# Optimization experiments

Hardware: AMD Instinct MI355X
Metric: run time of the kernel (lower is better)

## Reference

```python
import jax, jax.numpy as jnp
import numpy as np

NUM_HEAD = 16
DIM = 1024
T, B = 2048, 4


def setup_inputs() -> dict:
    key = jax.random.key(0)
    ks = jax.random.split(key, 12)
    s = 1.0 / np.sqrt(DIM)
    return {
        "x1": jax.random.normal(ks[0], (T, B, DIM), jnp.float32),
        "x2": jax.random.normal(ks[1], (T, B, DIM), jnp.float32),
        "Wq": jax.random.normal(ks[2], (DIM, DIM), jnp.float32) * s,
        "bq": jax.random.normal(ks[3], (DIM,), jnp.float32) * 0.01,
        "Wk": jax.random.normal(ks[4], (DIM, DIM), jnp.float32) * s,
        "bk": jax.random.normal(ks[5], (DIM,), jnp.float32) * 0.01,
        "Wv": jax.random.normal(ks[6], (DIM, DIM), jnp.float32) * s,
        "bv": jax.random.normal(ks[7], (DIM,), jnp.float32) * 0.01,
        "Wu": jax.random.normal(ks[8], (DIM, DIM), jnp.float32) * s,
        "bu": jax.random.normal(ks[9], (DIM,), jnp.float32) * 0.01,
    }


def reference(x1, x2, Wq, bq, Wk, bk, Wv, bv, Wu, bu):
    T1, B1, C = x1.shape
    T2 = x2.shape[0]
    H = NUM_HEAD
    hd = C // H
    # (T,B,C) -> (B,T,C)
    x1b = jnp.transpose(x1, (1, 0, 2))
    x2b = jnp.transpose(x2, (1, 0, 2))
    # torch Linear: y = x @ W.T + b
    q = (x1b @ Wq.T + bq).reshape(B1, T1, H, hd).transpose(0, 2, 1, 3)  # (B,H,T1,hd)
    k = (x2b @ Wk.T + bk).reshape(B1, T2, H, hd).transpose(0, 2, 1, 3)
    v = (x2b @ Wv.T + bv).reshape(B1, T2, H, hd).transpose(0, 2, 1, 3)
    # NOTE: source scales by 1/sqrt(C) (full dim), not 1/sqrt(head_dim)
    attn = jnp.einsum("bhqd,bhkd->bhqk", q, k) / jnp.sqrt(jnp.asarray(C, q.dtype))
    attn = jax.nn.softmax(attn, axis=-1)
    # dropout = identity (eval mode, deterministic reference)
    out = jnp.einsum("bhqk,bhkd->bhqd", attn, v)  # (B,H,T1,hd)
    out = out.transpose(0, 2, 1, 3).reshape(B1, T1, C)  # merge heads
    out = out @ Wu.T + bu
    return out
```

## Files before the change

### kernel.cpp

```cpp
#include <hip/hip_runtime.h>

#define TSEQ 2048
#define BB 4
#define CDIM 1024
#define NH 16
#define HD 64
#define MR (TSEQ*BB)
#define C2SCALE 0.045084220f

typedef __attribute__((ext_vector_type(8))) short sh8;
typedef __attribute__((ext_vector_type(4))) short sh4;
typedef __attribute__((ext_vector_type(4))) float f4;
typedef __attribute__((ext_vector_type(4))) unsigned int u32x4;

__device__ __forceinline__ unsigned short f2bf(float x){
  unsigned u = __builtin_bit_cast(unsigned, x);
  u += 0x7fffu + ((u>>16)&1u);
  return (unsigned short)(u>>16);
}

__device__ __forceinline__ unsigned pk2(float a, float b){
  unsigned ua = __builtin_bit_cast(unsigned, a) + 0x8000u;
  unsigned ub = __builtin_bit_cast(unsigned, b) + 0x8000u;
  return __builtin_amdgcn_perm(ua, ub, 0x07060302u);
}

__device__ __forceinline__ void gll16(const unsigned short* g, unsigned short* l){
  __builtin_amdgcn_global_load_lds(
      (const __attribute__((address_space(1))) unsigned int*)g,
      (__attribute__((address_space(3))) unsigned int*)l, 16, 0, 0);
}

__global__ void conv_x(const float* __restrict__ a, const float* __restrict__ b,
                       unsigned short* __restrict__ ya, unsigned short* __restrict__ yb){
  const float* s = blockIdx.y ? b : a;
  unsigned short* d = blockIdx.y ? yb : ya;
  int i = (blockIdx.x*256 + threadIdx.x)*4;
  f4 v = *(const f4*)(s+i);
  sh4 o;
  o.x = (short)f2bf(v.x); o.y = (short)f2bf(v.y);
  o.z = (short)f2bf(v.z); o.w = (short)f2bf(v.w);
  *(sh4*)(d+i) = o;
}

__global__ void conv_w(const float* __restrict__ w0, const float* __restrict__ w1,
                       const float* __restrict__ w2, const float* __restrict__ w3,
                       unsigned short* __restrict__ y0, unsigned short* __restrict__ y1,
                       unsigned short* __restrict__ y2, unsigned short* __restrict__ y3){
  const float* s; unsigned short* d;
  switch(blockIdx.y){
    case 0: s=w0; d=y0; break;
    case 1: s=w1; d=y1; break;
    case 2: s=w2; d=y2; break;
    default: s=w3; d=y3; break;
  }
  int i = (blockIdx.x*256 + threadIdx.x)*4;
  f4 v = *(const f4*)(s+i);
  sh4 o;
  o.x = (short)f2bf(v.x); o.y = (short)f2bf(v.y);
  o.z = (short)f2bf(v.z); o.w = (short)f2bf(v.w);
  *(sh4*)(d+i) = o;
}

#define NKT 16
#define BUFS 24576

__device__ __forceinline__ void gemm_core(
    const unsigned short* __restrict__ Aglob, const unsigned short* __restrict__ Bglob,
    unsigned short* smem, int m0, int n0, int tid, f4 (&acc)[4][4])
{
  const int wave = tid>>6, lane = tid&63;
  const int g = lane>>4, c = lane&15;
  const int wr = wave>>1, wc = wave&1;

  const unsigned short* aSrc[4]; int aOff[4];
  const unsigned short* bSrc[2]; int bOff[2];
#pragma unroll
  for (int i=0;i<4;i++){
    int slot = i*512+tid; int row = slot>>3, ch = slot&7;
    aSrc[i] = Aglob + (size_t)(m0+row)*CDIM + (ch^(row&7))*8;
    aOff[i] = slot*8;
  }
#pragma unroll
  for (int i=0;i<2;i++){
    int slot = i*512+tid; int row = slot>>3, ch = slot&7;
    bSrc[i] = Bglob + (size_t)(n0+row)*CDIM + (ch^(row&7))*8;
    bOff[i] = 16384 + slot*8;
  }
  const int arow = wr*64 + c;
  const int brow = wc*64 + c;
  const int ch0 = g ^ (c&7);
  const int ch1 = (4+g) ^ (c&7);

#pragma unroll
  for (int i=0;i<4;i++) gll16(aSrc[i],     smem + aOff[i]);
#pragma unroll
  for (int i=0;i<2;i++) gll16(bSrc[i],     smem + bOff[i]);
#pragma unroll
  for (int i=0;i<4;i++) gll16(aSrc[i]+64,  smem + BUFS + aOff[i]);
#pragma unroll
  for (int i=0;i<2;i++) gll16(bSrc[i]+64,  smem + BUFS + bOff[i]);
  asm volatile("s_waitcnt vmcnt(6)" ::: "memory");
  __builtin_amdgcn_s_barrier();
  __builtin_amdgcn_sched_barrier(0);

  int q = 0;
  for (int kt=0; kt<NKT; kt++){
    unsigned short* bufc = smem + q*BUFS;
    int r = q+2; if (r>=3) r-=3;
    unsigned short* dst = smem + r*BUFS;
    const int koff = (kt+2)*64;
    sh8 af[4][2], bfr[2][2];
#pragma unroll
    for (int mt=0;mt<4;mt++){
      af[mt][0] = *(const sh8*)(bufc + (arow+mt*16)*64 + ch0*8);
      af[mt][1] = *(const sh8*)(bufc + (arow+mt*16)*64 + ch1*8);
    }
#pragma unroll
    for (int nt=0;nt<2;nt++){
      bfr[nt][0] = *(const sh8*)(bufc + 16384 + (brow+nt*16)*64 + ch0*8);
      bfr[nt][1] = *(const sh8*)(bufc + 16384 + (brow+nt*16)*64 + ch1*8);
    }
    if (kt+2 < NKT){
#pragma unroll
      for (int i=0;i<4;i++) gll16(aSrc[i]+koff, dst + aOff[i]);
    }
    __builtin_amdgcn_s_barrier();
    __builtin_amdgcn_sched_barrier(0);
    __builtin_amdgcn_s_setprio(1);
#pragma unroll
    for (int mt=0;mt<4;mt++)
#pragma unroll
      for (int nt=0;nt<2;nt++){
        acc[mt][nt] = __builtin_amdgcn_mfma_f32_16x16x32_bf16(af[mt][0], bfr[nt][0], acc[mt][nt],0,0,0);
        acc[mt][nt] = __builtin_amdgcn_mfma_f32_16x16x32_bf16(af[mt][1], bfr[nt][1], acc[mt][nt],0,0,0);
      }
    __builtin_amdgcn_s_setprio(0);
    __builtin_amdgcn_s_barrier();
    __builtin_amdgcn_sched_barrier(0);
#pragma unroll
    for (int nt=0;nt<2;nt++){
      bfr[nt][0] = *(const sh8*)(bufc + 16384 + (brow+(nt+2)*16)*64 + ch0*8);
      bfr[nt][1] = *(const sh8*)(bufc + 16384 + (brow+(nt+2)*16)*64 + ch1*8);
    }
    if (kt+2 < NKT){
#pragma unroll
      for (int i=0;i<2;i++) gll16(bSrc[i]+koff, dst + bOff[i]);
    }
    __builtin_amdgcn_s_barrier();
    __builtin_amdgcn_sched_barrier(0);
    __builtin_amdgcn_s_setprio(1);
#pragma unroll
    for (int mt=0;mt<4;mt++)
#pragma unroll
      for (int nt=0;nt<2;nt++){
        acc[mt][nt+2] = __builtin_amdgcn_mfma_f32_16x16x32_bf16(af[mt][0], bfr[nt][0], acc[mt][nt+2],0,0,0);
        acc[mt][nt+2] = __builtin_amdgcn_mfma_f32_16x16x32_bf16(af[mt][1], bfr[nt][1], acc[mt][nt+2],0,0,0);
      }
    __builtin_amdgcn_s_setprio(0);
    if (kt < NKT-1){
      if (kt < NKT-2) asm volatile("s_waitcnt vmcnt(6)" ::: "memory");
      else            asm volatile("s_waitcnt vmcnt(0)" ::: "memory");
    }
    __builtin_amdgcn_s_barrier();
    __builtin_amdgcn_sched_barrier(0);
    q = (q==2)?0:q+1;
  }
}

__global__ __launch_bounds__(512,2) void gemm_u(
    const unsigned short* __restrict__ A, const unsigned short* __restrict__ Bw,
    const float* __restrict__ bias, float* __restrict__ Cout){
  __shared__ unsigned short smem[3*BUFS];
  const int tid  = threadIdx.x;
  const int wave = tid>>6, lane = tid&63;
  const int g = lane>>4, c = lane&15;
  const int m0 = blockIdx.x*256, n0 = blockIdx.y*128;
  const int wr = wave>>1, wc = wave&1;
  f4 acc[4][4] = {};
  gemm_core(A, Bw, smem, m0, n0, tid, acc);

#pragma unroll
  for (int nt=0; nt<4; nt++){
    int nn = n0 + wc*64 + nt*16 + c;
    float bsv = bias[nn];
#pragma unroll
    for (int mt=0; mt<4; mt++){
      int mb = m0 + wr*64 + mt*16 + 4*g;
#pragma unroll
      for (int r=0; r<4; r++)
        Cout[(size_t)(mb+r)*CDIM + nn] = acc[mt][nt][r] + bsv;
    }
  }
}

__global__ __launch_bounds__(512,2) void gemm_qkv(
    const unsigned short* __restrict__ x1b, const unsigned short* __restrict__ x2b,
    const unsigned short* __restrict__ wq, const unsigned short* __restrict__ wk,
    const unsigned short* __restrict__ wv,
    const float* __restrict__ bq, const float* __restrict__ bk, const float* __restrict__ bv,
    unsigned short* __restrict__ Qo, unsigned short* __restrict__ Ko,
    unsigned short* __restrict__ Vo){
  __shared__ unsigned short smem[3*BUFS];
  const int z = blockIdx.z;
  const unsigned short* A  = (z==0) ? x1b : x2b;
  const unsigned short* Bw = (z==0) ? wq : (z==1) ? wk : wv;
  const float* bias        = (z==0) ? bq : (z==1) ? bk : bv;
  const int tid  = threadIdx.x;
  const int wave = tid>>6, lane = tid&63;
  const int g = lane>>4, c = lane&15;
  const int m0 = blockIdx.x*256, n0 = blockIdx.y*128;
  const int wr = wave>>1, wc = wave&1;
  f4 acc[4][4] = {};
  gemm_core(A, Bw, smem, m0, n0, tid, acc);

#pragma unroll
  for (int nt=0; nt<4; nt++){
    int nn = n0 + wc*64 + nt*16 + c;
    float bsv = bias[nn];
#pragma unroll
    for (int mt=0; mt<4; mt++){
      int mb = m0 + wr*64 + mt*16 + 4*g;
#pragma unroll
      for (int r=0; r<4; r++){
        float v = acc[mt][nt][r] + bsv;
        int mm = mb + r;
        if (z==0){
          Qo[(size_t)mm*CDIM + nn] = f2bf(v*C2SCALE);
        } else if (z==1){
          Ko[(size_t)mm*CDIM + nn] = f2bf(v);
        } else {
          int t = mm>>2, bb = mm&3, h = nn>>6, d = nn&63;
          Vo[(((size_t)bb*NH + h)*HD + d)*TSEQ + t] = f2bf(v);
        }
      }
    }
  }
}

__global__ __launch_bounds__(256,3) void attn_kernel(
    const unsigned short* __restrict__ Q, const unsigned short* __restrict__ Kb,
    const unsigned short* __restrict__ Vt, unsigned short* __restrict__ O){
  __shared__ unsigned short Ks[128*64];
  __shared__ unsigned short Vs[64*128];
  const int tid=threadIdx.x, wave=tid>>6, lane=tid&63;
  const int g=lane>>4, c=lane&15;
  const bool godd = (g&1);
  const int gx = blockIdx.x;
  const int bh = ((gx>>7)<<3) | (gx&7);
  const int qt = (gx>>3)&15;
  const int b = bh>>4, h = bh&15;
  const int qbase = qt*128 + wave*32;

  const unsigned short* kbase[4];
  const unsigned short* vbase[4];
#pragma unroll
  for (int i=0; i<4; i++){
    int cc = i*256+tid;
    int krow = cc>>3, kch = (cc&7) ^ (krow&7);
    kbase[i] = Kb + ((size_t)krow*BB + b)*CDIM + h*HD + kch*8;
    int vd = cc>>4, vch = (cc&15) ^ (vd&15);
    vbase[i] = Vt + ((size_t)(b*NH+h)*HD + vd)*TSEQ + vch*8;
  }

  sh8 qfr[2][2];
#pragma unroll
  for (int qf=0; qf<2; qf++)
#pragma unroll
    for (int kc=0; kc<2; kc++){
      int t = qbase + qf*16 + c;
      qfr[qf][kc] = *(const sh8*)(Q + ((size_t)t*BB + b)*CDIM + h*HD + kc*32 + g*8);
    }

  f4 oacc[4][2] = {};
  float lrun[2] = {0.f, 0.f};

  f4 kreg[4], vreg[4];
#pragma unroll
  for (int i=0; i<4; i++){
    kreg[i] = *(const f4*)(kbase[i]);
    vreg[i] = *(const f4*)(vbase[i]);
  }
#pragma unroll
  for (int i=0; i<4; i++){
    *(f4*)(Ks + (i*256+tid)*8) = kreg[i];
    *(f4*)(Vs + (i*256+tid)*8) = vreg[i];
  }
  __syncthreads();

  for (int iter=0; iter<TSEQ/128; iter++){
    if (iter < TSEQ/128-1){
      int k0n = (iter+1)*128;
#pragma unroll
      for (int i=0; i<4; i++){
        kreg[i] = *(const f4*)(kbase[i] + (size_t)k0n*BB*CDIM);
        vreg[i] = *(const f4*)(vbase[i] + k0n);
      }
    }

#pragma unroll
    for (int half=0; half<2; half++){
      f4 sacc[4][2] = {};
      __builtin_amdgcn_s_setprio(1);
#pragma unroll
      for (int kfl=0; kfl<4; kfl++){
        int kf = half*4 + kfl;
        sh8 af[2];
#pragma unroll
        for (int kc=0; kc<2; kc++){
          int ch = (kc*4+g) ^ (c&7);
          af[kc] = *(const sh8*)(Ks + (kf*16+c)*64 + ch*8);
        }
#pragma unroll
        for (int kc=0; kc<2; kc++)
#pragma unroll
          for (int qf=0; qf<2; qf++)
            sacc[kfl][qf] = __builtin_amdgcn_mfma_f32_16x16x32_bf16(af[kc], qfr[qf][kc], sacc[kfl][qf],0,0,0);
      }
      __builtin_amdgcn_s_setprio(0);

#pragma unroll
      for (int kc2l=0; kc2l<2; kc2l++){
        const int kc2 = half*2 + kc2l;
        sh8 pf[2];
#pragma unroll
        for (int qf=0; qf<2; qf++){
          f4 sa = sacc[2*kc2l][qf];
          f4 sb = sacc[2*kc2l+1][qf];
          float pa0 = __builtin_amdgcn_exp2f(sa[0]);
          float pa1 = __builtin_amdgcn_exp2f(sa[1]);
          float pa2 = __builtin_amdgcn_exp2f(sa[2]);
          float pa3 = __builtin_amdgcn_exp2f(sa[3]);
          float pb0 = __builtin_amdgcn_exp2f(sb[0]);
          float pb1 = __builtin_amdgcn_exp2f(sb[1]);
          float pb2 = __builtin_amdgcn_exp2f(sb[2]);
          float pb3 = __builtin_amdgcn_exp2f(sb[3]);
          lrun[qf] += ((pa0+pa1)+(pa2+pa3)) + ((pb0+pb1)+(pb2+pb3));
          unsigned A0 = pk2(pa1, pa0);
          unsigned A1 = pk2(pa3, pa2);
          unsigned B0 = pk2(pb1, pb0);
          unsigned B1 = pk2(pb3, pb2);
          asm("v_permlane32_swap_b32 %0, %1" : "+v"(A0), "+v"(B0));
          asm("v_permlane32_swap_b32 %0, %1" : "+v"(A1), "+v"(B1));
          unsigned xA0 = (unsigned)__builtin_amdgcn_ds_swizzle((int)A0, 0x401F);
          unsigned xA1 = (unsigned)__builtin_amdgcn_ds_swizzle((int)A1, 0x401F);
          unsigned xB0 = (unsigned)__builtin_amdgcn_ds_swizzle((int)B0, 0x401F);
          unsigned xB1 = (unsigned)__builtin_amdgcn_ds_swizzle((int)B1, 0x401F);
          u32x4 pw;
          pw.x = godd ? xB0 : A0;
          pw.y = godd ? xB1 : A1;
          pw.z = godd ? B0  : xA0;
          pw.w = godd ? B1  : xA1;
          pf[qf] = __builtin_bit_cast(sh8, pw);
        }
        __builtin_amdgcn_s_setprio(1);
#pragma unroll
        for (int df=0; df<4; df++){
          int ch = (kc2*4+g) ^ c;
          sh8 vf = *(const sh8*)(Vs + (df*16+c)*128 + ch*8);
#pragma unroll
          for (int qf=0; qf<2; qf++)
            oacc[df][qf] = __builtin_amdgcn_mfma_f32_16x16x32_bf16(vf, pf[qf], oacc[df][qf],0,0,0);
        }
        __builtin_amdgcn_s_setprio(0);
      }
    }

    __syncthreads();
    if (iter < TSEQ/128-1){
#pragma unroll
      for (int i=0; i<4; i++){
        *(f4*)(Ks + (i*256+tid)*8) = kreg[i];
        *(f4*)(Vs + (i*256+tid)*8) = vreg[i];
      }
      __syncthreads();
    }
  }

#pragma unroll
  for (int qf=0; qf<2; qf++){
    lrun[qf] += __shfl_xor(lrun[qf], 16, 64);
    lrun[qf] += __shfl_xor(lrun[qf], 32, 64);
    float inv = 1.0f/lrun[qf];
    int t = qbase + qf*16 + c;
#pragma unroll
    for (int df=0; df<4; df++){
      uint2 pr;
      pr.x = pk2(oacc[df][qf][1]*inv, oacc[df][qf][0]*inv);
      pr.y = pk2(oacc[df][qf][3]*inv, oacc[df][qf][2]*inv);
      *(uint2*)(O + ((size_t)b*TSEQ + t)*CDIM + h*HD + df*16 + 4*g) = pr;
    }
  }
}

extern "C" void kernel_launch(void* const* d_in, const int* in_sizes, int n_in,
                              void* d_out, int out_size, void* d_ws, size_t ws_size,
                              hipStream_t stream){
  (void)in_sizes; (void)n_in; (void)out_size; (void)ws_size;
  const float* x1 = (const float*)d_in[0];
  const float* x2 = (const float*)d_in[1];
  const float* Wq = (const float*)d_in[2];
  const float* bq = (const float*)d_in[3];
  const float* Wk = (const float*)d_in[4];
  const float* bk = (const float*)d_in[5];
  const float* Wv = (const float*)d_in[6];
  const float* bv = (const float*)d_in[7];
  const float* Wu = (const float*)d_in[8];
  const float* bu = (const float*)d_in[9];

  unsigned short* ws = (unsigned short*)d_ws;
  size_t o = 0;
  unsigned short* x1b = ws + o; o += (size_t)MR*CDIM;
  unsigned short* x2b = ws + o; o += (size_t)MR*CDIM;
  unsigned short* wqb = ws + o; o += (size_t)CDIM*CDIM;
  unsigned short* wkb = ws + o; o += (size_t)CDIM*CDIM;
  unsigned short* wvb = ws + o; o += (size_t)CDIM*CDIM;
  unsigned short* wub = ws + o; o += (size_t)CDIM*CDIM;
  unsigned short* Qb  = ws + o; o += (size_t)MR*CDIM;
  unsigned short* Kbf = ws + o; o += (size_t)MR*CDIM;
  unsigned short* Vtb = ws + o; o += (size_t)MR*CDIM;
  unsigned short* Ob  = x1b;

  conv_x<<<dim3((MR*CDIM)/1024, 2),   256, 0, stream>>>(x1, x2, x1b, x2b);
  conv_w<<<dim3((CDIM*CDIM)/1024, 4), 256, 0, stream>>>(Wq, Wk, Wv, Wu, wqb, wkb, wvb, wub);

  gemm_qkv<<<dim3(MR/256, CDIM/128, 3), 512, 0, stream>>>(
      x1b, x2b, wqb, wkb, wvb, bq, bk, bv, Qb, Kbf, Vtb);
  attn_kernel<<<dim3(1024), 256, 0, stream>>>(Qb, Kbf, Vtb, Ob);
  gemm_u<<<dim3(MR/256, CDIM/128), 512, 0, stream>>>(Ob, wub, bu, (float*)d_out);
}
```

Baseline: 330.6 us.

## Double-buffer attention K/V tiles with direct global-to-LDS loads, drop GEMM sched barriers

The attention kernel now works on 64-key tiles held in two LDS buffers. Each next tile is fetched with asynchronous global-to-LDS loads (gll16) instead of being staged through registers and written back. This removes one barrier per tile and the register pressure of staging, and the smaller LDS footprint lets launch bounds allow 4 blocks per CU. The GEMM core also drops its sched_barrier calls so the compiler can interleave instructions across the block barriers. In exchange, completion of the asynchronous loads is now implied by __syncthreads rather than an explicit vmcnt wait, and the scheduling freedom in the GEMM could disturb the hand-tuned interleaving.

```diff
diff --git a/kernel.cpp b/kernel.cpp
--- a/kernel.cpp
+++ b/kernel.cpp
@@ -102,7 +102,6 @@
   for (int i=0;i<2;i++) gll16(bSrc[i]+64,  smem + BUFS + bOff[i]);
   asm volatile("s_waitcnt vmcnt(6)" ::: "memory");
   __builtin_amdgcn_s_barrier();
-  __builtin_amdgcn_sched_barrier(0);
 
   int q = 0;
   for (int kt=0; kt<NKT; kt++){
@@ -126,7 +125,6 @@
       for (int i=0;i<4;i++) gll16(aSrc[i]+koff, dst + aOff[i]);
     }
     __builtin_amdgcn_s_barrier();
-    __builtin_amdgcn_sched_barrier(0);
     __builtin_amdgcn_s_setprio(1);
 #pragma unroll
     for (int mt=0;mt<4;mt++)
@@ -137,7 +135,6 @@
       }
     __builtin_amdgcn_s_setprio(0);
     __builtin_amdgcn_s_barrier();
-    __builtin_amdgcn_sched_barrier(0);
 #pragma unroll
     for (int nt=0;nt<2;nt++){
       bfr[nt][0] = *(const sh8*)(bufc + 16384 + (brow+(nt+2)*16)*64 + ch0*8);
@@ -148,7 +145,6 @@
       for (int i=0;i<2;i++) gll16(bSrc[i]+koff, dst + bOff[i]);
     }
     __builtin_amdgcn_s_barrier();
-    __builtin_amdgcn_sched_barrier(0);
     __builtin_amdgcn_s_setprio(1);
 #pragma unroll
     for (int mt=0;mt<4;mt++)
@@ -163,7 +159,6 @@
       else            asm volatile("s_waitcnt vmcnt(0)" ::: "memory");
     }
     __builtin_amdgcn_s_barrier();
-    __builtin_amdgcn_sched_barrier(0);
     q = (q==2)?0:q+1;
   }
 }
@@ -238,11 +233,11 @@
   }
 }
 
-__global__ __launch_bounds__(256,3) void attn_kernel(
+__global__ __launch_bounds__(256,4) void attn_kernel(
     const unsigned short* __restrict__ Q, const unsigned short* __restrict__ Kb,
     const unsigned short* __restrict__ Vt, unsigned short* __restrict__ O){
-  __shared__ unsigned short Ks[128*64];
-  __shared__ unsigned short Vs[64*128];
+  __shared__ unsigned short Ks[2][64*64];
+  __shared__ unsigned short Vs[2][64*64];
   const int tid=threadIdx.x, wave=tid>>6, lane=tid&63;
   const int g=lane>>4, c=lane&15;
   const bool godd = (g&1);
@@ -252,15 +247,15 @@
   const int b = bh>>4, h = bh&15;
   const int qbase = qt*128 + wave*32;
 
-  const unsigned short* kbase[4];
-  const unsigned short* vbase[4];
-#pragma unroll
-  for (int i=0; i<4; i++){
+  const unsigned short* kb0[2];
+  const unsigned short* vb0[2];
+#pragma unroll
+  for (int i=0; i<2; i++){
     int cc = i*256+tid;
     int krow = cc>>3, kch = (cc&7) ^ (krow&7);
-    kbase[i] = Kb + ((size_t)krow*BB + b)*CDIM + h*HD + kch*8;
-    int vd = cc>>4, vch = (cc&15) ^ (vd&15);
-    vbase[i] = Vt + ((size_t)(b*NH+h)*HD + vd)*TSEQ + vch*8;
+    kb0[i] = Kb + ((size_t)krow*BB + b)*CDIM + h*HD + kch*8;
+    int vd = cc>>3, vch = (cc&7) ^ (vd&7);
+    vb0[i] = Vt + ((size_t)(b*NH+h)*HD + vd)*TSEQ + vch*8;
   }
 
   sh8 qfr[2][2];
@@ -275,106 +270,93 @@
   f4 oacc[4][2] = {};
   float lrun[2] = {0.f, 0.f};
 
-  f4 kreg[4], vreg[4];
-#pragma unroll
-  for (int i=0; i<4; i++){
-    kreg[i] = *(const f4*)(kbase[i]);
-    vreg[i] = *(const f4*)(vbase[i]);
-  }
-#pragma unroll
-  for (int i=0; i<4; i++){
-    *(f4*)(Ks + (i*256+tid)*8) = kreg[i];
-    *(f4*)(Vs + (i*256+tid)*8) = vreg[i];
+#pragma unroll
+  for (int i=0; i<2; i++){
+    gll16(kb0[i], Ks[0] + (i*256+tid)*8);
+    gll16(vb0[i], Vs[0] + (i*256+tid)*8);
   }
   __syncthreads();
 
-  for (int iter=0; iter<TSEQ/128; iter++){
-    if (iter < TSEQ/128-1){
-      int k0n = (iter+1)*128;
-#pragma unroll
-      for (int i=0; i<4; i++){
-        kreg[i] = *(const f4*)(kbase[i] + (size_t)k0n*BB*CDIM);
-        vreg[i] = *(const f4*)(vbase[i] + k0n);
-      }
-    }
-
-#pragma unroll
-    for (int half=0; half<2; half++){
-      f4 sacc[4][2] = {};
+  const int NT = TSEQ/64;
+  int cur = 0;
+  for (int it=0; it<NT; it++){
+    if (it+1 < NT){
+      int k0n = (it+1)*64;
+#pragma unroll
+      for (int i=0; i<2; i++){
+        gll16(kb0[i] + (size_t)k0n*BB*CDIM, Ks[cur^1] + (i*256+tid)*8);
+        gll16(vb0[i] + k0n,                 Vs[cur^1] + (i*256+tid)*8);
+      }
+    }
+    const unsigned short* ks = Ks[cur];
+    const unsigned short* vs = Vs[cur];
+
+#pragma unroll
+    for (int sub=0; sub<2; sub++){
+      f4 sacc[2][2] = {};
       __builtin_amdgcn_s_setprio(1);
 #pragma unroll
-      for (int kfl=0; kfl<4; kfl++){
-        int kf = half*4 + kfl;
+      for (int j=0; j<2; j++){
+        int kf = sub*2 + j;
         sh8 af[2];
 #pragma unroll
         for (int kc=0; kc<2; kc++){
           int ch = (kc*4+g) ^ (c&7);
-          af[kc] = *(const sh8*)(Ks + (kf*16+c)*64 + ch*8);
+          af[kc] = *(const sh8*)(ks + (kf*16+c)*64 + ch*8);
         }
 #pragma unroll
         for (int kc=0; kc<2; kc++)
 #pragma unroll
           for (int qf=0; qf<2; qf++)
-            sacc[kfl][qf] = __builtin_amdgcn_mfma_f32_16x16x32_bf16(af[kc], qfr[qf][kc], sacc[kfl][qf],0,0,0);
+            sacc[j][qf] = __builtin_amdgcn_mfma_f32_16x16x32_bf16(af[kc], qfr[qf][kc], sacc[j][qf],0,0,0);
       }
       __builtin_amdgcn_s_setprio(0);
 
-#pragma unroll
-      for (int kc2l=0; kc2l<2; kc2l++){
-        const int kc2 = half*2 + kc2l;
-        sh8 pf[2];
-#pragma unroll
-        for (int qf=0; qf<2; qf++){
-          f4 sa = sacc[2*kc2l][qf];
-          f4 sb = sacc[2*kc2l+1][qf];
-          float pa0 = __builtin_amdgcn_exp2f(sa[0]);
-          float pa1 = __builtin_amdgcn_exp2f(sa[1]);
-          float pa2 = __builtin_amdgcn_exp2f(sa[2]);
-          float pa3 = __builtin_amdgcn_exp2f(sa[3]);
-          float pb0 = __builtin_amdgcn_exp2f(sb[0]);
-          float pb1 = __builtin_amdgcn_exp2f(sb[1]);
-          float pb2 = __builtin_amdgcn_exp2f(sb[2]);
-          float pb3 = __builtin_amdgcn_exp2f(sb[3]);
-          lrun[qf] += ((pa0+pa1)+(pa2+pa3)) + ((pb0+pb1)+(pb2+pb3));
-          unsigned A0 = pk2(pa1, pa0);
-          unsigned A1 = pk2(pa3, pa2);
-          unsigned B0 = pk2(pb1, pb0);
-          unsigned B1 = pk2(pb3, pb2);
-          asm("v_permlane32_swap_b32 %0, %1" : "+v"(A0), "+v"(B0));
-          asm("v_permlane32_swap_b32 %0, %1" : "+v"(A1), "+v"(B1));
-          unsigned xA0 = (unsigned)__builtin_amdgcn_ds_swizzle((int)A0, 0x401F);
-          unsigned xA1 = (unsigned)__builtin_amdgcn_ds_swizzle((int)A1, 0x401F);
-          unsigned xB0 = (unsigned)__builtin_amdgcn_ds_swizzle((int)B0, 0x401F);
-          unsigned xB1 = (unsigned)__builtin_amdgcn_ds_swizzle((int)B1, 0x401F);
-          u32x4 pw;
-          pw.x = godd ? xB0 : A0;
-          pw.y = godd ? xB1 : A1;
-          pw.z = godd ? B0  : xA0;
-          pw.w = godd ? B1  : xA1;
-          pf[qf] = __builtin_bit_cast(sh8, pw);
-        }
-        __builtin_amdgcn_s_setprio(1);
-#pragma unroll
-        for (int df=0; df<4; df++){
-          int ch = (kc2*4+g) ^ c;
-          sh8 vf = *(const sh8*)(Vs + (df*16+c)*128 + ch*8);
-#pragma unroll
-          for (int qf=0; qf<2; qf++)
-            oacc[df][qf] = __builtin_amdgcn_mfma_f32_16x16x32_bf16(vf, pf[qf], oacc[df][qf],0,0,0);
-        }
-        __builtin_amdgcn_s_setprio(0);
-      }
+      sh8 pf[2];
+#pragma unroll
+      for (int qf=0; qf<2; qf++){
+        f4 sa = sacc[0][qf];
+        f4 sb = sacc[1][qf];
+        float pa0 = __builtin_amdgcn_exp2f(sa[0]);
+        float pa1 = __builtin_amdgcn_exp2f(sa[1]);
+        float pa2 = __builtin_amdgcn_exp2f(sa[2]);
+        float pa3 = __builtin_amdgcn_exp2f(sa[3]);
+        float pb0 = __builtin_amdgcn_exp2f(sb[0]);
+        float pb1 = __builtin_amdgcn_exp2f(sb[1]);
+        float pb2 = __builtin_amdgcn_exp2f(sb[2]);
+        float pb3 = __builtin_amdgcn_exp2f(sb[3]);
+        lrun[qf] += ((pa0+pa1)+(pa2+pa3)) + ((pb0+pb1)+(pb2+pb3));
+        unsigned A0 = pk2(pa1, pa0);
+        unsigned A1 = pk2(pa3, pa2);
+        unsigned B0 = pk2(pb1, pb0);
+        unsigned B1 = pk2(pb3, pb2);
+        asm("v_permlane32_swap_b32 %0, %1" : "+v"(A0), "+v"(B0));
+        asm("v_permlane32_swap_b32 %0, %1" : "+v"(A1), "+v"(B1));
+        unsigned xA0 = (unsigned)__builtin_amdgcn_ds_swizzle((int)A0, 0x401F);
+        unsigned xA1 = (unsigned)__builtin_amdgcn_ds_swizzle((int)A1, 0x401F);
+        unsigned xB0 = (unsigned)__builtin_amdgcn_ds_swizzle((int)B0, 0x401F);
+        unsigned xB1 = (unsigned)__builtin_amdgcn_ds_swizzle((int)B1, 0x401F);
+        u32x4 pw;
+        pw.x = godd ? xB0 : A0;
+        pw.y = godd ? xB1 : A1;
+        pw.z = godd ? B0  : xA0;
+        pw.w = godd ? B1  : xA1;
+        pf[qf] = __builtin_bit_cast(sh8, pw);
+      }
+      __builtin_amdgcn_s_setprio(1);
+#pragma unroll
+      for (int df=0; df<4; df++){
+        int ch = (sub*4+g) ^ (c&7);
+        sh8 vf = *(const sh8*)(vs + (df*16+c)*64 + ch*8);
+#pragma unroll
+        for (int qf=0; qf<2; qf++)
+          oacc[df][qf] = __builtin_amdgcn_mfma_f32_16x16x32_bf16(vf, pf[qf], oacc[df][qf],0,0,0);
+      }
+      __builtin_amdgcn_s_setprio(0);
     }
 
     __syncthreads();
-    if (iter < TSEQ/128-1){
-#pragma unroll
-      for (int i=0; i<4; i++){
-        *(f4*)(Ks + (i*256+tid)*8) = kreg[i];
-        *(f4*)(Vs + (i*256+tid)*8) = vreg[i];
-      }
-      __syncthreads();
-    }
+    cur ^= 1;
   }
 
 #pragma unroll
```

After: 318.8 us. 3.6% less time.
